# Performance work log

Measured on AMD Instinct MI355X. Metric: run time of the kernel, lower is better.

The kernel has to match this reference:

```python
import jax, jax.numpy as jnp
import numpy as np

ATTN_MASK_VALUE = -1e10
N, D_IN, D_HEAD, D_OUT = 8192, 1024, 128, 1024


def setup_inputs() -> dict:
    key = jax.random.key(0)
    k_x, k_wqkv, k_bqkv, k_wo, k_bo = jax.random.split(key, 5)
    x = jax.random.normal(k_x, (N, D_IN), dtype=jnp.float32)
    # flax Dense default: lecun_normal kernel, zeros bias; use scaled normal for test
    w_qkv = jax.random.normal(k_wqkv, (D_IN, 3 * D_HEAD), dtype=jnp.float32) / np.sqrt(D_IN)
    b_qkv = jnp.zeros((3 * D_HEAD,), dtype=jnp.float32)
    w_out = jax.random.normal(k_wo, (D_HEAD, D_OUT), dtype=jnp.float32) / np.sqrt(D_HEAD)
    b_out = jnp.zeros((D_OUT,), dtype=jnp.float32)
    return {"x": x, "w_qkv": w_qkv, "b_qkv": b_qkv, "w_out": w_out, "b_out": b_out}


def reference(x, w_qkv, b_qkv, w_out, b_out):
    n = x.shape[0]
    scale = D_HEAD ** (-0.5)
    qkv = x @ w_qkv + b_qkv                      # [n, 3*dh]
    q, k, v = jnp.split(qkv, 3, axis=-1)         # each [n, dh]
    sim = jnp.einsum('id,jd->ij', q, k) * scale  # [n, n]
    mask = jnp.triu(jnp.ones((n, n), dtype=bool), 1)
    sim = jnp.where(mask, ATTN_MASK_VALUE, sim)
    attn = jax.nn.softmax(sim, axis=-1)
    out = jnp.einsum('ij,jd->id', attn, v)       # [n, dh]
    return out @ w_out + b_out                   # [n, d_out]
```

## Files before the change

### kernel.cpp

```cpp
#include <hip/hip_runtime.h>
#include <stdint.h>

typedef __attribute__((ext_vector_type(4))) float f32x4;
typedef __attribute__((ext_vector_type(8))) __bf16 bf16x8;

#define MFMA16(a, b, c) __builtin_amdgcn_mfma_f32_16x16x32_bf16(a, b, c, 0, 0, 0)
#define GLOAD16(g, l)                                                              \
  __builtin_amdgcn_global_load_lds(                                                \
      (const __attribute__((address_space(1))) unsigned int*)(g),                  \
      (__attribute__((address_space(3))) unsigned int*)(l), 16, 0, 0)
#define EXP2F(x) __builtin_amdgcn_exp2f(x)

static __device__ __forceinline__ unsigned short f2b(float f) {
  unsigned int u = __float_as_uint(f);
  u += 0x7fff + ((u >> 16) & 1);
  return (unsigned short)(u >> 16);
}

#define NROWS 8192
#define DIN   1024
#define DH    128
#define DOUT  1024

__global__ void k_convert_w(const float* __restrict__ wqkv, const float* __restrict__ wout,
                            unsigned short* __restrict__ wqkvT, unsigned short* __restrict__ woutT) {
  __shared__ float t[64][65];
  const int bid = blockIdx.x;
  const float* src;
  unsigned short* dst;
  int k0, n0, sstride, dstride;
  if (bid < 96) {
    int kt = bid / 6, nt = bid % 6;
    k0 = kt * 64; n0 = nt * 64;
    src = wqkv; sstride = 384; dst = wqkvT; dstride = 1024;
  } else {
    int b2 = bid - 96;
    int kt = b2 & 1, nt = b2 >> 1;
    k0 = kt * 64; n0 = nt * 64;
    src = wout; sstride = 1024; dst = woutT; dstride = 128;
  }
  const int tid = threadIdx.x;
  const int r = tid >> 4, c4 = (tid & 15) * 4;
#pragma unroll
  for (int j = 0; j < 4; ++j) {
    int rr = r + j * 16;
    float4 v = *reinterpret_cast<const float4*>(src + (size_t)(k0 + rr) * sstride + n0 + c4);
    t[rr][c4 + 0] = v.x; t[rr][c4 + 1] = v.y; t[rr][c4 + 2] = v.z; t[rr][c4 + 3] = v.w;
  }
  __syncthreads();
#pragma unroll
  for (int j = 0; j < 4; ++j) {
    int rn = r + j * 16;
    ushort4 h;
    h.x = f2b(t[c4 + 0][rn]); h.y = f2b(t[c4 + 1][rn]);
    h.z = f2b(t[c4 + 2][rn]); h.w = f2b(t[c4 + 3][rn]);
    *reinterpret_cast<ushort4*>(dst + (size_t)(n0 + rn) * dstride + k0 + c4) = h;
  }
}

__global__ void k_convert_x(const float* __restrict__ x, unsigned short* __restrict__ xb) {
  int i = (blockIdx.x * 256 + threadIdx.x) * 4;
  float4 v = *reinterpret_cast<const float4*>(x + i);
  ushort4 h;
  h.x = f2b(v.x); h.y = f2b(v.y); h.z = f2b(v.z); h.w = f2b(v.w);
  *reinterpret_cast<ushort4*>(xb + i) = h;
}

__launch_bounds__(256, 2)
__global__ void k_qkv_gemm(const unsigned short* __restrict__ xb, const unsigned short* __restrict__ wT,
                           const float* __restrict__ bqkv,
                           unsigned short* __restrict__ Qb, unsigned short* __restrict__ Kb,
                           unsigned short* __restrict__ Vb) {
  const int hb = blockIdx.x;
  const int xcd = hb & 7, jj = hb >> 3;
  const int tau = xcd * 24 + jj;
  const int bn = tau % 3, bm = tau / 3;
  const int tid = threadIdx.x;
  const int lane = tid & 63, w = tid >> 6;
  const int l15 = lane & 15, g = lane >> 4;
  const int wm = (w >> 1) * 64, wn = (w & 1) * 64;
  const int row0 = bm * 128, col0 = bn * 128;

  __shared__ __align__(16) char Ash[2][16384];
  __shared__ __align__(16) char Bsh[2][16384];

  f32x4 acc[4][4] = {};

#define QKV_STAGE(k0, buf)                                                          \
  {                                                                                 \
    _Pragma("unroll")                                                               \
    for (int j2 = 0; j2 < 4; ++j2) {                                                \
      int idx = j2 * 256 + tid;                                                     \
      int r = idx >> 3, gg = idx & 7, sgg = gg ^ (r & 7);                           \
      GLOAD16(xb + (size_t)(row0 + r) * DIN + (k0) + sgg * 8, Ash[buf] + idx * 16); \
      GLOAD16(wT + (size_t)(col0 + r) * DIN + (k0) + sgg * 8, Bsh[buf] + idx * 16); \
    }                                                                               \
  }

  QKV_STAGE(0, 0);
  __syncthreads();
  int cur = 0;
  for (int k0 = 0; k0 < DIN; k0 += 64) {
    if (k0 + 64 < DIN) QKV_STAGE(k0 + 64, cur ^ 1);
#pragma unroll
    for (int ksl = 0; ksl < 2; ++ksl) {
      bf16x8 af[4], bfr[4];
#pragma unroll
      for (int i = 0; i < 4; ++i) {
        int r = wm + i * 16 + l15;
        int ba = r * 128 + ksl * 64 + g * 16;
        af[i] = *reinterpret_cast<bf16x8*>(Ash[cur] + (ba ^ ((r & 7) << 4)));
        int n = wn + i * 16 + l15;
        int bb = n * 128 + ksl * 64 + g * 16;
        bfr[i] = *reinterpret_cast<bf16x8*>(Bsh[cur] + (bb ^ ((n & 7) << 4)));
      }
#pragma unroll
      for (int i = 0; i < 4; ++i)
#pragma unroll
        for (int jn = 0; jn < 4; ++jn)
          acc[i][jn] = MFMA16(af[i], bfr[jn], acc[i][jn]);
    }
    __syncthreads();
    cur ^= 1;
  }

  unsigned short* outb = (bn == 0) ? Qb : (bn == 1 ? Kb : Vb);
#pragma unroll
  for (int i = 0; i < 4; ++i)
#pragma unroll
    for (int jn = 0; jn < 4; ++jn)
#pragma unroll
      for (int r = 0; r < 4; ++r) {
        int grow = row0 + wm + i * 16 + g * 4 + r;
        int lcol = wn + jn * 16 + l15;
        float vv = acc[i][jn][r] + bqkv[bn * 128 + lcol];
        outb[(size_t)grow * DH + lcol] = f2b(vv);
      }
}

__global__ void k_transpose_v(const unsigned short* __restrict__ V, unsigned short* __restrict__ VT) {
  __shared__ __align__(16) unsigned short t[64 * 128];
  const int b = blockIdx.x;
  const int tid = threadIdx.x;
  const int kv0 = b * 64;
#pragma unroll
  for (int j = 0; j < 4; ++j) {
    int c = j * 256 + tid;
    int r = c >> 4, cc = (c & 15) * 8;
    uint4 v = *reinterpret_cast<const uint4*>(V + (size_t)(kv0 + r) * DH + cc);
    int col = (cc + ((r >> 3) & 7) * 8) & 127;
    *reinterpret_cast<uint4*>(&t[r * 128 + col]) = v;
  }
  __syncthreads();
#pragma unroll
  for (int j = 0; j < 4; ++j) {
    int c = j * 256 + tid;
    int d = c >> 3, kk = (c & 7) * 8;
    unsigned short tmp[8];
#pragma unroll
    for (int e = 0; e < 8; ++e) {
      int r = kk + e;
      int col = (d + ((r >> 3) & 7) * 8) & 127;
      tmp[e] = t[r * 128 + col];
    }
    *reinterpret_cast<uint4*>(VT + (size_t)d * NROWS + kv0 + kk) = *reinterpret_cast<uint4*>(tmp);
  }
}

__launch_bounds__(256, 2)
__global__ void k_flash(const unsigned short* __restrict__ Q, const unsigned short* __restrict__ Kg,
                        const unsigned short* __restrict__ VT,
                        float* __restrict__ Opart, float* __restrict__ MLpart, int LQ) {
  const int ci = blockIdx.x;
  const int t = (int)(gridDim.y - 1) - (int)blockIdx.y;
  const int Jq = 1 << LQ;
  if (ci * Jq > t) return;
  const int qb = t << 7;
  const int ks = ci * (Jq << 7);
  const int ke = min(ks + (Jq << 7), qb + 128);
  const int nsteps = (ke - ks) >> 6;

  const int a = t >> LQ, b = t & (Jq - 1);
  const int slot = t + ((Jq * a * (a - 1)) >> 1) + a * b + ci;

  const int tid = threadIdx.x;
  const int lane = tid & 63, w = tid >> 6;
  const int l15 = lane & 15, g = lane >> 4;

  __shared__ __align__(16) char Ksh[2][16384];
  __shared__ __align__(16) char Vsh[2][16384];
  __shared__ __align__(16) char Psh[4][4096];

  const int qr0 = qb + w * 16 + l15;
  const int qr1 = qr0 + 64;
  bf16x8 qf0[4], qf1[4];
#pragma unroll
  for (int d = 0; d < 4; ++d) {
    qf0[d] = *reinterpret_cast<const bf16x8*>(Q + (size_t)qr0 * DH + d * 32 + g * 8);
    qf1[d] = *reinterpret_cast<const bf16x8*>(Q + (size_t)qr1 * DH + d * 32 + g * 8);
  }

  f32x4 acco0[8] = {}, acco1[8] = {};
  float m0 = -1e30f, l0 = 0.f, m1 = -1e30f, l1 = 0.f;
  const float c2 = 0.08838834764831843f * 1.4426950408889634f;

#define FL_STAGE(kv0, buf)                                                            \
  {                                                                                   \
    _Pragma("unroll")                                                                 \
    for (int j2 = 0; j2 < 4; ++j2) {                                                  \
      int idx = j2 * 256 + tid;                                                       \
      int r = idx >> 4, gg = idx & 15, sgg = gg ^ (r & 7);                            \
      GLOAD16(Kg + (size_t)((kv0) + r) * DH + sgg * 8, Ksh[buf] + idx * 16);          \
    }                                                                                 \
    _Pragma("unroll")                                                                 \
    for (int j2 = 0; j2 < 4; ++j2) {                                                  \
      int idx = j2 * 256 + tid;                                                       \
      int d = idx >> 3, gg = idx & 7, sgg = gg ^ (d & 7);                             \
      GLOAD16(VT + (size_t)d * NROWS + (kv0) + sgg * 8, Vsh[buf] + idx * 16);         \
    }                                                                                 \
  }

  char* Pw = Psh[w];

  FL_STAGE(ks, 0);
  __syncthreads();
  int cur = 0;

  for (int s = 0; s < nsteps; ++s) {
    const int kv0 = ks + (s << 6);
    if (s + 1 < nsteps) FL_STAGE(kv0 + 64, cur ^ 1);
    const bool act0 = (kv0 < qb + 64);

    f32x4 accs0[4] = {}, accs1[4] = {};
    if (act0) {
#pragma unroll
      for (int jc = 0; jc < 4; ++jc)
#pragma unroll
        for (int d = 0; d < 4; ++d) {
          int r = jc * 16 + l15;
          int byte = r * 256 + d * 64 + g * 16; byte ^= (r & 7) << 4;
          bf16x8 kf = *reinterpret_cast<bf16x8*>(Ksh[cur] + byte);
          accs1[jc] = MFMA16(kf, qf1[d], accs1[jc]);
          accs0[jc] = MFMA16(kf, qf0[d], accs0[jc]);
        }
    } else {
#pragma unroll
      for (int jc = 0; jc < 4; ++jc)
#pragma unroll
        for (int d = 0; d < 4; ++d) {
          int r = jc * 16 + l15;
          int byte = r * 256 + d * 64 + g * 16; byte ^= (r & 7) << 4;
          bf16x8 kf = *reinterpret_cast<bf16x8*>(Ksh[cur] + byte);
          accs1[jc] = MFMA16(kf, qf1[d], accs1[jc]);
        }
    }

#define SOFTMAX_PW(ACCS, ACCO, M, L, QROW, ROWBASE)                                   \
    {                                                                                 \
      float p[4][4];                                                                  \
      float mx = -3e38f;                                                              \
      _Pragma("unroll")                                                               \
      for (int jc = 0; jc < 4; ++jc)                                                  \
        _Pragma("unroll")                                                             \
        for (int r = 0; r < 4; ++r) {                                                 \
          float sv = ACCS[jc][r] * c2;                                                \
          int kk = kv0 + jc * 16 + (g << 2) + r;                                      \
          sv = (kk <= (QROW)) ? sv : -3e38f;                                          \
          p[jc][r] = sv;                                                              \
          mx = fmaxf(mx, sv);                                                         \
        }                                                                             \
      mx = fmaxf(mx, __shfl_xor(mx, 16));                                             \
      mx = fmaxf(mx, __shfl_xor(mx, 32));                                             \
      float mnew = fmaxf(M, mx);                                                      \
      float fac = EXP2F(M - mnew);                                                    \
      float ps = 0.f;                                                                 \
      _Pragma("unroll")                                                               \
      for (int jc = 0; jc < 4; ++jc)                                                  \
        _Pragma("unroll")                                                             \
        for (int r = 0; r < 4; ++r) {                                                 \
          float e = EXP2F(p[jc][r] - mnew);                                           \
          p[jc][r] = e; ps += e;                                                      \
        }                                                                             \
      ps += __shfl_xor(ps, 16);                                                       \
      ps += __shfl_xor(ps, 32);                                                       \
      L = L * fac + ps;                                                               \
      M = mnew;                                                                       \
      _Pragma("unroll")                                                               \
      for (int dc = 0; dc < 8; ++dc)                                                  \
        _Pragma("unroll")                                                             \
        for (int r = 0; r < 4; ++r) ACCO[dc][r] *= fac;                               \
      int rq = (ROWBASE) + l15;                                                       \
      _Pragma("unroll")                                                               \
      for (int jc = 0; jc < 4; ++jc) {                                                \
        ushort4 pb;                                                                   \
        pb.x = f2b(p[jc][0]); pb.y = f2b(p[jc][1]);                                   \
        pb.z = f2b(p[jc][2]); pb.w = f2b(p[jc][3]);                                   \
        int byte = rq * 128 + jc * 32 + g * 8; byte ^= (rq & 7) << 4;                 \
        *reinterpret_cast<ushort4*>(Pw + byte) = pb;                                  \
      }                                                                               \
    }

    if (act0) SOFTMAX_PW(accs0, acco0, m0, l0, qr0, 0);
    SOFTMAX_PW(accs1, acco1, m1, l1, qr1, 16);
    __asm__ volatile("s_waitcnt lgkmcnt(0)" ::: "memory");
    __builtin_amdgcn_sched_barrier(0);

    bf16x8 pf1[2];
#pragma unroll
    for (int ks2 = 0; ks2 < 2; ++ks2) {
      int rq = 16 + l15;
      int byte = rq * 128 + ks2 * 64 + g * 16; byte ^= (rq & 7) << 4;
      pf1[ks2] = *reinterpret_cast<bf16x8*>(Pw + byte);
    }
    if (act0) {
      bf16x8 pf0[2];
#pragma unroll
      for (int ks2 = 0; ks2 < 2; ++ks2) {
        int byte = l15 * 128 + ks2 * 64 + g * 16; byte ^= (l15 & 7) << 4;
        pf0[ks2] = *reinterpret_cast<bf16x8*>(Pw + byte);
      }
#pragma unroll
      for (int dc = 0; dc < 8; ++dc) {
        int vr = dc * 16 + l15;
        int b0 = vr * 128 + g * 16; b0 ^= (vr & 7) << 4;
        bf16x8 vf0 = *reinterpret_cast<bf16x8*>(Vsh[cur] + b0);
        bf16x8 vf1 = *reinterpret_cast<bf16x8*>(Vsh[cur] + (b0 ^ 64));
        acco1[dc] = MFMA16(vf0, pf1[0], acco1[dc]);
        acco1[dc] = MFMA16(vf1, pf1[1], acco1[dc]);
        acco0[dc] = MFMA16(vf0, pf0[0], acco0[dc]);
        acco0[dc] = MFMA16(vf1, pf0[1], acco0[dc]);
      }
    } else {
#pragma unroll
      for (int dc = 0; dc < 8; ++dc) {
        int vr = dc * 16 + l15;
        int b0 = vr * 128 + g * 16; b0 ^= (vr & 7) << 4;
        bf16x8 vf0 = *reinterpret_cast<bf16x8*>(Vsh[cur] + b0);
        bf16x8 vf1 = *reinterpret_cast<bf16x8*>(Vsh[cur] + (b0 ^ 64));
        acco1[dc] = MFMA16(vf0, pf1[0], acco1[dc]);
        acco1[dc] = MFMA16(vf1, pf1[1], acco1[dc]);
      }
    }
    __syncthreads();
    cur ^= 1;
  }

  const size_t r0 = (size_t)slot * 128 + w * 16 + l15;
  const size_t r1 = r0 + 64;
#pragma unroll
  for (int dc = 0; dc < 8; ++dc) {
    f32x4 o0, o1;
#pragma unroll
    for (int r = 0; r < 4; ++r) { o0[r] = acco0[dc][r]; o1[r] = acco1[dc][r]; }
    *reinterpret_cast<f32x4*>(Opart + r0 * DH + dc * 16 + (g << 2)) = o0;
    *reinterpret_cast<f32x4*>(Opart + r1 * DH + dc * 16 + (g << 2)) = o1;
  }
  if (g == 0) {
    MLpart[r0 * 2 + 0] = m0;
    MLpart[r0 * 2 + 1] = l0;
    MLpart[r1 * 2 + 0] = m1;
    MLpart[r1 * 2 + 1] = l1;
  }
}

__global__ void k_merge(const float* __restrict__ Opart, const float* __restrict__ MLpart,
                        unsigned short* __restrict__ O, int LQ) {
  int tg = blockIdx.x * 256 + threadIdx.x;
  int row = tg >> 5, d4 = (tg & 31) * 4;
  int t = row >> 7;
  int Jq = 1 << LQ;
  int a = t >> LQ, b = t & (Jq - 1);
  int base = t + ((Jq * a * (a - 1)) >> 1) + a * b;
  int nc = a + 1;
  int rowin = row & 127;
  float M = -3e38f;
  for (int i = 0; i < nc; ++i) M = fmaxf(M, MLpart[((size_t)(base + i) * 128 + rowin) * 2]);
  float L = 0.f;
  f32x4 acc = {};
  for (int i = 0; i < nc; ++i) {
    size_t sr = (size_t)(base + i) * 128 + rowin;
    float mi = MLpart[sr * 2];
    float li = MLpart[sr * 2 + 1];
    float wg = EXP2F(mi - M);
    L += li * wg;
    f32x4 o = *reinterpret_cast<const f32x4*>(Opart + sr * DH + d4);
#pragma unroll
    for (int e = 0; e < 4; ++e) acc[e] += wg * o[e];
  }
  float inv = 1.f / L;
  ushort4 hv;
  hv.x = f2b(acc[0] * inv); hv.y = f2b(acc[1] * inv);
  hv.z = f2b(acc[2] * inv); hv.w = f2b(acc[3] * inv);
  *reinterpret_cast<ushort4*>(O + (size_t)row * DH + d4) = hv;
}

__launch_bounds__(256, 2)
__global__ void k_out_gemm(const unsigned short* __restrict__ O, const unsigned short* __restrict__ wT,
                           const float* __restrict__ bout, float* __restrict__ out) {
  const int hb = blockIdx.x;
  const int xcd = hb & 7, jj = hb >> 3;
  const int tau = xcd * 256 + jj;
  const int bn = tau & 15, bm = tau >> 4;
  const int tid = threadIdx.x;
  const int lane = tid & 63, w = tid >> 6;
  const int l15 = lane & 15, g = lane >> 4;
  const int wm = (w >> 1) * 32, wn = (w & 1) * 32;
  const int row0 = bm * 64, col0 = bn * 64;

  __shared__ __align__(16) char Ash[16384];
  __shared__ __align__(16) char Bsh[16384];

#pragma unroll
  for (int j = 0; j < 4; ++j) {
    int idx = j * 256 + tid;
    int r = idx >> 4, gg = idx & 15;
    int sgg = gg ^ (r & 7);
    GLOAD16(O + (size_t)(row0 + r) * DH + sgg * 8, Ash + idx * 16);
    GLOAD16(wT + (size_t)(col0 + r) * DH + sgg * 8, Bsh + idx * 16);
  }
  __syncthreads();

  f32x4 acc[2][2] = {};
#pragma unroll
  for (int ksl = 0; ksl < 4; ++ksl) {
    bf16x8 af[2], bfr[2];
#pragma unroll
    for (int i = 0; i < 2; ++i) {
      int r = wm + i * 16 + l15;
      int ba = r * 256 + ksl * 64 + g * 16;
      af[i] = *reinterpret_cast<bf16x8*>(Ash + (ba ^ ((r & 7) << 4)));
      int n = wn + i * 16 + l15;
      int bb = n * 256 + ksl * 64 + g * 16;
      bfr[i] = *reinterpret_cast<bf16x8*>(Bsh + (bb ^ ((n & 7) << 4)));
    }
#pragma unroll
    for (int i = 0; i < 2; ++i)
#pragma unroll
      for (int jn = 0; jn < 2; ++jn)
        acc[i][jn] = MFMA16(af[i], bfr[jn], acc[i][jn]);
  }

#pragma unroll
  for (int i = 0; i < 2; ++i)
#pragma unroll
    for (int jn = 0; jn < 2; ++jn)
#pragma unroll
      for (int r = 0; r < 4; ++r) {
        int grow = row0 + wm + i * 16 + g * 4 + r;
        int gcol = col0 + wn + jn * 16 + l15;
        out[(size_t)grow * DOUT + gcol] = acc[i][jn][r] + bout[gcol];
      }
}

extern "C" void kernel_launch(void* const* d_in, const int* in_sizes, int n_in,
                              void* d_out, int out_size, void* d_ws, size_t ws_size,
                              hipStream_t stream) {
  const float* x    = (const float*)d_in[0];
  const float* wqkv = (const float*)d_in[1];
  const float* bqkv = (const float*)d_in[2];
  const float* wout = (const float*)d_in[3];
  const float* bout = (const float*)d_in[4];
  float* out = (float*)d_out;

  size_t fixed = 786432 + 262144 + (size_t)NROWS * DIN * 2 + (size_t)5 * NROWS * DH * 2;
  int LQ = 2;
  size_t slots = 0;
  for (; LQ <= 6; ++LQ) {
    int Jq = 1 << LQ, A = 64 / Jq;
    slots = (size_t)Jq * A * (A + 1) / 2;
    size_t need = fixed + slots * ((size_t)128 * DH * 4 + 128 * 8);
    if (need <= ws_size || LQ == 6) break;
  }

  char* ws = (char*)d_ws;
  size_t off = 0;
  unsigned short* wqkvT = (unsigned short*)(ws + off); off += (size_t)384 * 1024 * 2;
  unsigned short* woutT = (unsigned short*)(ws + off); off += (size_t)1024 * 128 * 2;
  unsigned short* xb  = (unsigned short*)(ws + off); off += (size_t)NROWS * DIN * 2;
  unsigned short* Qb  = (unsigned short*)(ws + off); off += (size_t)NROWS * DH * 2;
  unsigned short* Kb  = (unsigned short*)(ws + off); off += (size_t)NROWS * DH * 2;
  unsigned short* Vb  = (unsigned short*)(ws + off); off += (size_t)NROWS * DH * 2;
  unsigned short* VTb = (unsigned short*)(ws + off); off += (size_t)NROWS * DH * 2;
  unsigned short* Ob  = (unsigned short*)(ws + off); off += (size_t)NROWS * DH * 2;
  float* Opart  = (float*)(ws + off); off += slots * (size_t)128 * DH * 4;
  float* MLpart = (float*)(ws + off); off += slots * (size_t)128 * 8;

  k_convert_w<<<128, 256, 0, stream>>>(wqkv, wout, wqkvT, woutT);
  k_convert_x<<<(NROWS * DIN) / 1024, 256, 0, stream>>>(x, xb);
  k_qkv_gemm<<<192, 256, 0, stream>>>(xb, wqkvT, bqkv, Qb, Kb, Vb);
  k_transpose_v<<<128, 256, 0, stream>>>(Vb, VTb);
  k_flash<<<dim3(64 >> LQ, 64), 256, 0, stream>>>(Qb, Kb, VTb, Opart, MLpart, LQ);
  k_merge<<<(NROWS * 32) / 256, 256, 0, stream>>>(Opart, MLpart, Ob, LQ);
  k_out_gemm<<<2048, 256, 0, stream>>>(Ob, woutT, bout, out);
}
```

Measured before the change: 115.9 us.

## Single-buffer flash LDS with register prefetch, bf16 partials, finer KV split

The flash kernel now prefetches the next K/V tile into registers during compute and writes it to single-buffered LDS after a barrier, halving LDS use in place of the async global-to-LDS double buffer. Partial outputs are stored as bf16 instead of fp32, halving partial-output traffic in flash and merge. The split search starts at LQ=1, allowing smaller KV chunks and more blocks when workspace permits. This adds an extra barrier per step and register pressure, and bf16 partials lose some precision before merging.

```diff
diff --git a/kernel.cpp b/kernel.cpp
--- a/kernel.cpp
+++ b/kernel.cpp
@@ -15,6 +15,10 @@
   unsigned int u = __float_as_uint(f);
   u += 0x7fff + ((u >> 16) & 1);
   return (unsigned short)(u >> 16);
+}
+static __device__ __forceinline__ float b2f(unsigned short h) {
+  unsigned int u = ((unsigned int)h) << 16;
+  return __uint_as_float(u);
 }
 
 #define NROWS 8192
@@ -170,7 +174,7 @@
 __launch_bounds__(256, 2)
 __global__ void k_flash(const unsigned short* __restrict__ Q, const unsigned short* __restrict__ Kg,
                         const unsigned short* __restrict__ VT,
-                        float* __restrict__ Opart, float* __restrict__ MLpart, int LQ) {
+                        unsigned short* __restrict__ Opart, float* __restrict__ MLpart, int LQ) {
   const int ci = blockIdx.x;
   const int t = (int)(gridDim.y - 1) - (int)blockIdx.y;
   const int Jq = 1 << LQ;
@@ -187,8 +191,8 @@
   const int lane = tid & 63, w = tid >> 6;
   const int l15 = lane & 15, g = lane >> 4;
 
-  __shared__ __align__(16) char Ksh[2][16384];
-  __shared__ __align__(16) char Vsh[2][16384];
+  __shared__ __align__(16) char Ksh[16384];
+  __shared__ __align__(16) char Vsh[16384];
   __shared__ __align__(16) char Psh[4][4096];
 
   const int qr0 = qb + w * 16 + l15;
@@ -204,31 +208,43 @@
   float m0 = -1e30f, l0 = 0.f, m1 = -1e30f, l1 = 0.f;
   const float c2 = 0.08838834764831843f * 1.4426950408889634f;
 
-#define FL_STAGE(kv0, buf)                                                            \
-  {                                                                                   \
-    _Pragma("unroll")                                                                 \
-    for (int j2 = 0; j2 < 4; ++j2) {                                                  \
-      int idx = j2 * 256 + tid;                                                       \
-      int r = idx >> 4, gg = idx & 15, sgg = gg ^ (r & 7);                            \
-      GLOAD16(Kg + (size_t)((kv0) + r) * DH + sgg * 8, Ksh[buf] + idx * 16);          \
-    }                                                                                 \
-    _Pragma("unroll")                                                                 \
-    for (int j2 = 0; j2 < 4; ++j2) {                                                  \
-      int idx = j2 * 256 + tid;                                                       \
-      int d = idx >> 3, gg = idx & 7, sgg = gg ^ (d & 7);                             \
-      GLOAD16(VT + (size_t)d * NROWS + (kv0) + sgg * 8, Vsh[buf] + idx * 16);         \
-    }                                                                                 \
-  }
-
   char* Pw = Psh[w];
 
-  FL_STAGE(ks, 0);
+#pragma unroll
+  for (int j2 = 0; j2 < 4; ++j2) {
+    int idx = j2 * 256 + tid;
+    int r = idx >> 4, gg = idx & 15, sgg = gg ^ (r & 7);
+    GLOAD16(Kg + (size_t)(ks + r) * DH + sgg * 8, Ksh + idx * 16);
+  }
+#pragma unroll
+  for (int j2 = 0; j2 < 4; ++j2) {
+    int idx = j2 * 256 + tid;
+    int d = idx >> 3, gg = idx & 7, sgg = gg ^ (d & 7);
+    GLOAD16(VT + (size_t)d * NROWS + ks + sgg * 8, Vsh + idx * 16);
+  }
   __syncthreads();
-  int cur = 0;
 
   for (int s = 0; s < nsteps; ++s) {
     const int kv0 = ks + (s << 6);
-    if (s + 1 < nsteps) FL_STAGE(kv0 + 64, cur ^ 1);
+    const bool pre = (s + 1 < nsteps);
+
+    uint4 kreg[4], vreg[4];
+    if (pre) {
+      const int kv1 = kv0 + 64;
+#pragma unroll
+      for (int j2 = 0; j2 < 4; ++j2) {
+        int idx = j2 * 256 + tid;
+        int r = idx >> 4, gg = idx & 15, sgg = gg ^ (r & 7);
+        kreg[j2] = *reinterpret_cast<const uint4*>(Kg + (size_t)(kv1 + r) * DH + sgg * 8);
+      }
+#pragma unroll
+      for (int j2 = 0; j2 < 4; ++j2) {
+        int idx = j2 * 256 + tid;
+        int d = idx >> 3, gg = idx & 7, sgg = gg ^ (d & 7);
+        vreg[j2] = *reinterpret_cast<const uint4*>(VT + (size_t)d * NROWS + kv1 + sgg * 8);
+      }
+    }
+
     const bool act0 = (kv0 < qb + 64);
 
     f32x4 accs0[4] = {}, accs1[4] = {};
@@ -239,7 +255,7 @@
         for (int d = 0; d < 4; ++d) {
           int r = jc * 16 + l15;
           int byte = r * 256 + d * 64 + g * 16; byte ^= (r & 7) << 4;
-          bf16x8 kf = *reinterpret_cast<bf16x8*>(Ksh[cur] + byte);
+          bf16x8 kf = *reinterpret_cast<bf16x8*>(Ksh + byte);
           accs1[jc] = MFMA16(kf, qf1[d], accs1[jc]);
           accs0[jc] = MFMA16(kf, qf0[d], accs0[jc]);
         }
@@ -250,7 +266,7 @@
         for (int d = 0; d < 4; ++d) {
           int r = jc * 16 + l15;
           int byte = r * 256 + d * 64 + g * 16; byte ^= (r & 7) << 4;
-          bf16x8 kf = *reinterpret_cast<bf16x8*>(Ksh[cur] + byte);
+          bf16x8 kf = *reinterpret_cast<bf16x8*>(Ksh + byte);
           accs1[jc] = MFMA16(kf, qf1[d], accs1[jc]);
         }
     }
@@ -323,8 +339,8 @@
       for (int dc = 0; dc < 8; ++dc) {
         int vr = dc * 16 + l15;
         int b0 = vr * 128 + g * 16; b0 ^= (vr & 7) << 4;
-        bf16x8 vf0 = *reinterpret_cast<bf16x8*>(Vsh[cur] + b0);
-        bf16x8 vf1 = *reinterpret_cast<bf16x8*>(Vsh[cur] + (b0 ^ 64));
+        bf16x8 vf0 = *reinterpret_cast<bf16x8*>(Vsh + b0);
+        bf16x8 vf1 = *reinterpret_cast<bf16x8*>(Vsh + (b0 ^ 64));
         acco1[dc] = MFMA16(vf0, pf1[0], acco1[dc]);
         acco1[dc] = MFMA16(vf1, pf1[1], acco1[dc]);
         acco0[dc] = MFMA16(vf0, pf0[0], acco0[dc]);
@@ -335,25 +351,36 @@
       for (int dc = 0; dc < 8; ++dc) {
         int vr = dc * 16 + l15;
         int b0 = vr * 128 + g * 16; b0 ^= (vr & 7) << 4;
-        bf16x8 vf0 = *reinterpret_cast<bf16x8*>(Vsh[cur] + b0);
-        bf16x8 vf1 = *reinterpret_cast<bf16x8*>(Vsh[cur] + (b0 ^ 64));
+        bf16x8 vf0 = *reinterpret_cast<bf16x8*>(Vsh + b0);
+        bf16x8 vf1 = *reinterpret_cast<bf16x8*>(Vsh + (b0 ^ 64));
         acco1[dc] = MFMA16(vf0, pf1[0], acco1[dc]);
         acco1[dc] = MFMA16(vf1, pf1[1], acco1[dc]);
       }
     }
+
     __syncthreads();
-    cur ^= 1;
+    if (pre) {
+#pragma unroll
+      for (int j2 = 0; j2 < 4; ++j2) {
+        int idx = j2 * 256 + tid;
+        *reinterpret_cast<uint4*>(Ksh + idx * 16) = kreg[j2];
+        *reinterpret_cast<uint4*>(Vsh + idx * 16) = vreg[j2];
+      }
+      __syncthreads();
+    }
   }
 
   const size_t r0 = (size_t)slot * 128 + w * 16 + l15;
   const size_t r1 = r0 + 64;
 #pragma unroll
   for (int dc = 0; dc < 8; ++dc) {
-    f32x4 o0, o1;
-#pragma unroll
-    for (int r = 0; r < 4; ++r) { o0[r] = acco0[dc][r]; o1[r] = acco1[dc][r]; }
-    *reinterpret_cast<f32x4*>(Opart + r0 * DH + dc * 16 + (g << 2)) = o0;
-    *reinterpret_cast<f32x4*>(Opart + r1 * DH + dc * 16 + (g << 2)) = o1;
+    ushort4 o0, o1;
+    o0.x = f2b(acco0[dc][0]); o0.y = f2b(acco0[dc][1]);
+    o0.z = f2b(acco0[dc][2]); o0.w = f2b(acco0[dc][3]);
+    o1.x = f2b(acco1[dc][0]); o1.y = f2b(acco1[dc][1]);
+    o1.z = f2b(acco1[dc][2]); o1.w = f2b(acco1[dc][3]);
+    *reinterpret_cast<ushort4*>(Opart + r0 * DH + dc * 16 + (g << 2)) = o0;
+    *reinterpret_cast<ushort4*>(Opart + r1 * DH + dc * 16 + (g << 2)) = o1;
   }
   if (g == 0) {
     MLpart[r0 * 2 + 0] = m0;
@@ -363,7 +390,7 @@
   }
 }
 
-__global__ void k_merge(const float* __restrict__ Opart, const float* __restrict__ MLpart,
+__global__ void k_merge(const unsigned short* __restrict__ Opart, const float* __restrict__ MLpart,
                         unsigned short* __restrict__ O, int LQ) {
   int tg = blockIdx.x * 256 + threadIdx.x;
   int row = tg >> 5, d4 = (tg & 31) * 4;
@@ -383,9 +410,9 @@
     float li = MLpart[sr * 2 + 1];
     float wg = EXP2F(mi - M);
     L += li * wg;
-    f32x4 o = *reinterpret_cast<const f32x4*>(Opart + sr * DH + d4);
-#pragma unroll
-    for (int e = 0; e < 4; ++e) acc[e] += wg * o[e];
+    ushort4 o = *reinterpret_cast<const ushort4*>(Opart + sr * DH + d4);
+    acc[0] += wg * b2f(o.x); acc[1] += wg * b2f(o.y);
+    acc[2] += wg * b2f(o.z); acc[3] += wg * b2f(o.w);
   }
   float inv = 1.f / L;
   ushort4 hv;
@@ -463,12 +490,12 @@
   float* out = (float*)d_out;
 
   size_t fixed = 786432 + 262144 + (size_t)NROWS * DIN * 2 + (size_t)5 * NROWS * DH * 2;
-  int LQ = 2;
+  int LQ = 1;
   size_t slots = 0;
   for (; LQ <= 6; ++LQ) {
     int Jq = 1 << LQ, A = 64 / Jq;
     slots = (size_t)Jq * A * (A + 1) / 2;
-    size_t need = fixed + slots * ((size_t)128 * DH * 4 + 128 * 8);
+    size_t need = fixed + slots * ((size_t)128 * DH * 2 + 128 * 8);
     if (need <= ws_size || LQ == 6) break;
   }
 
@@ -482,7 +509,7 @@
   unsigned short* Vb  = (unsigned short*)(ws + off); off += (size_t)NROWS * DH * 2;
   unsigned short* VTb = (unsigned short*)(ws + off); off += (size_t)NROWS * DH * 2;
   unsigned short* Ob  = (unsigned short*)(ws + off); off += (size_t)NROWS * DH * 2;
-  float* Opart  = (float*)(ws + off); off += slots * (size_t)128 * DH * 4;
+  unsigned short* Opart = (unsigned short*)(ws + off); off += slots * (size_t)128 * DH * 2;
   float* MLpart = (float*)(ws + off); off += slots * (size_t)128 * 8;
 
   k_convert_w<<<128, 256, 0, stream>>>(wqkv, wout, wqkvT, woutT);
```

New measurement: 158.7 us. 36.9% more time.
